# Optimization experiments

Hardware: AMD Instinct MI355X
Metric: run time of the kernel (lower is better)

The kernel has to match this reference:

```python
import jax, jax.numpy as jnp
import numpy as np

B, N, M, K = 128, 20000, 85400, 3  # trajectories, variables, clauses, literals/clause


def setup_inputs() -> dict:
    key = jax.random.key(0)
    k_v, k_idx, k_sign, k_xs = jax.random.split(key, 4)
    v = jax.random.normal(k_v, (B, N), dtype=jnp.float32)
    input_idx = jax.random.randint(k_idx, (B, M, K), 0, N, dtype=jnp.int32)
    # literal signs are exactly +/-1
    input_sign = jnp.where(jax.random.normal(k_sign, (B, M, K)) > 0, 1.0, -1.0).astype(jnp.float32)
    xl = jnp.ones((B, M), dtype=jnp.float32)            # long-term memory (init 1)
    xs = jax.random.uniform(k_xs, (B, M), dtype=jnp.float32)  # short-term memory in [0,1]
    # [alpha, beta, gamma, delta, epsilon, zeta] -- typical MemComputing coefficients
    param = jnp.array([5.0, 20.0, 0.25, 0.05, 0.001, 0.1], dtype=jnp.float32)
    return {"v": v, "xl": xl, "xs": xs, "param": param,
            "input_sign": input_sign, "input_idx": input_idx}


def reference(v, xl, xs, param, input_sign, input_idx):
    """Faithful port of OR.calc_grad. Returns (C, grad_v, dxl, dxs)."""
    b = v.shape[0]
    k = input_idx.shape[-1]
    alpha, beta, gamma, delta, epsilon, zeta = param
    b_idx = jnp.arange(b)[:, None, None]                # (B,1,1)
    inp = v[b_idx, input_idx] * input_sign              # (B,M,K) gather + sign
    v_top, v_top_idx = jax.lax.top_k(inp, 2)            # top-2 literal values per clause
    v_top = (1.0 - v_top) * 0.5                         # transform; v_top[...,0] is smallest -> C
    C = v_top[..., 0]                                   # (B,M) clause 'distance to satisfied'
    hot = jax.nn.one_hot(v_top_idx[..., 0], k, dtype=v.dtype)  # (B,M,K) mask of max literal
    # G: C everywhere, second-best value at the max-literal slot, scaled by xl*xs
    G = jnp.where(hot > 0, v_top[..., 1:2], C[..., None]) * (xl * xs)[..., None]
    # R: C only at the max-literal slot, scaled by (1+zeta*xl)*(1-xs)
    R = hot * C[..., None] * ((1.0 + zeta * xl) * (1.0 - xs))[..., None]
    dv = -(G + R) * input_sign                          # (B,M,K)
    grad_v = jnp.zeros_like(v).at[b_idx, input_idx].add(dv)  # scatter-add over dim 1
    dxl = -alpha * (C - delta)                          # (B,M)
    dxs = -beta * (xs + epsilon) * (C - gamma)          # (B,M)
    return C, grad_v, dxl, dxs
```

## Files before the change

kernel.cpp:

```cpp
#include <hip/hip_runtime.h>


#define NMAX 20000
#define BPB  4

typedef int   int4v   __attribute__((ext_vector_type(4)));
typedef float float4v __attribute__((ext_vector_type(4)));

__device__ __forceinline__ void clause_math(
    float a0, float a1, float a2, float xlv, float xsv, float zeta,
    float& C, float& g0, float& g1, float& g2)
{
    int k0; float m0, m1;
    if (a0 >= a1) {
        if (a0 >= a2) { k0 = 0; m0 = a0; m1 = fmaxf(a1, a2); }
        else          { k0 = 2; m0 = a2; m1 = fmaxf(a0, a1); }
    } else {
        if (a1 >= a2) { k0 = 1; m0 = a1; m1 = fmaxf(a0, a2); }
        else          { k0 = 2; m0 = a2; m1 = fmaxf(a0, a1); }
    }
    C = (1.f - m0) * 0.5f;
    const float T2 = (1.f - m1) * 0.5f;
    const float gl = xlv * xsv;
    const float rC = C * ((1.f + zeta * xlv) * (1.f - xsv));
    g0 = (k0 == 0 ? T2 : C) * gl + (k0 == 0 ? rC : 0.f);
    g1 = (k0 == 1 ? T2 : C) * gl + (k0 == 1 ? rC : 0.f);
    g2 = (k0 == 2 ? T2 : C) * gl + (k0 == 2 ? rC : 0.f);
}

__global__ __launch_bounds__(1024, 8) void or_priv3(
    const float* __restrict__ v,
    const float* __restrict__ xl,
    const float* __restrict__ xs,
    const float* __restrict__ param,
    const float* __restrict__ sign,
    const int*   __restrict__ idx,
    float* __restrict__ outC,
    float* __restrict__ outdxl,
    float* __restrict__ outdxs,
    float* __restrict__ partial,
    int N, int M, int B, int chunk)
{
    __shared__ float sg[NMAX];

    const int id  = blockIdx.x;
    const int cpx = gridDim.x >> 3;
    const int cid = (id & 7) * cpx + (id >> 3);
    const int b   = cid >> 2;
    const int j   = cid & 3;
    const int tid = threadIdx.x;

    {
        float4v* sg4 = (float4v*)sg;
        const float4v z = {0.f, 0.f, 0.f, 0.f};
        const int n4 = N >> 2;
        for (int i = tid; i < n4; i += 1024) sg4[i] = z;
        for (int i = (n4 << 2) + tid; i < N; i += 1024) sg[i] = 0.f;
    }
    __syncthreads();

    const float alpha = param[0], beta = param[1], gamma = param[2];
    const float delta = param[3], eps  = param[4], zeta  = param[5];

    const float* __restrict__ vb = v + (size_t)b * N;

    const int mstart = j * chunk;
    const int mend   = min(M, mstart + chunk);
    const int ngroups = (mend > mstart) ? ((mend - mstart + 3) >> 2) : 0;

    for (int g = tid; g < ngroups; g += 1024) {
        const int m0 = mstart + (g << 2);
        const size_t base = (size_t)b * M + m0;

        if (m0 + 3 < mend) {
            const int4v*   __restrict__ ip = (const int4v*)(idx + base * 3);
            const float4v* __restrict__ sp = (const float4v*)(sign + base * 3);
            const int4v   ia = __builtin_nontemporal_load(ip + 0);
            const int4v   ib = __builtin_nontemporal_load(ip + 1);
            const int4v   ic = __builtin_nontemporal_load(ip + 2);
            const float4v sa = __builtin_nontemporal_load(sp + 0);
            const float4v sb = __builtin_nontemporal_load(sp + 1);
            const float4v sc = __builtin_nontemporal_load(sp + 2);
            const float4v xl4 = __builtin_nontemporal_load((const float4v*)(xl + base));
            const float4v xs4 = __builtin_nontemporal_load((const float4v*)(xs + base));

            const int   ii[12] = {ia.x, ia.y, ia.z, ia.w, ib.x, ib.y, ib.z, ib.w,
                                  ic.x, ic.y, ic.z, ic.w};
            const float ss[12] = {sa.x, sa.y, sa.z, sa.w, sb.x, sb.y, sb.z, sb.w,
                                  sc.x, sc.y, sc.z, sc.w};
            const float xlA[4] = {xl4.x, xl4.y, xl4.z, xl4.w};
            const float xsA[4] = {xs4.x, xs4.y, xs4.z, xs4.w};
            float Cv[4], dxlv[4], dxsv[4];

            #pragma unroll
            for (int c = 0; c < 4; ++c) {
                const int   i0 = ii[3*c], i1 = ii[3*c+1], i2 = ii[3*c+2];
                const float s0 = ss[3*c], s1 = ss[3*c+1], s2 = ss[3*c+2];
                const float a0 = vb[i0] * s0, a1 = vb[i1] * s1, a2 = vb[i2] * s2;
                float C, g0, g1, g2;
                clause_math(a0, a1, a2, xlA[c], xsA[c], zeta, C, g0, g1, g2);
                unsafeAtomicAdd(&sg[i0], -g0 * s0);
                unsafeAtomicAdd(&sg[i1], -g1 * s1);
                unsafeAtomicAdd(&sg[i2], -g2 * s2);
                Cv[c]   = C;
                dxlv[c] = -alpha * (C - delta);
                dxsv[c] = -beta * (xsA[c] + eps) * (C - gamma);
            }
            const float4v cv  = {Cv[0], Cv[1], Cv[2], Cv[3]};
            const float4v lv  = {dxlv[0], dxlv[1], dxlv[2], dxlv[3]};
            const float4v svo = {dxsv[0], dxsv[1], dxsv[2], dxsv[3]};
            __builtin_nontemporal_store(cv,  (float4v*)(outC + base));
            __builtin_nontemporal_store(lv,  (float4v*)(outdxl + base));
            __builtin_nontemporal_store(svo, (float4v*)(outdxs + base));
        } else {
            for (int m = m0; m < mend; ++m) {
                const size_t bm  = (size_t)b * M + m;
                const size_t bm3 = bm * 3;
                const int   i0 = idx[bm3 + 0], i1 = idx[bm3 + 1], i2 = idx[bm3 + 2];
                const float s0 = sign[bm3 + 0], s1 = sign[bm3 + 1], s2 = sign[bm3 + 2];
                const float a0 = vb[i0] * s0, a1 = vb[i1] * s1, a2 = vb[i2] * s2;
                const float xlv = xl[bm], xsv = xs[bm];
                float C, g0, g1, g2;
                clause_math(a0, a1, a2, xlv, xsv, zeta, C, g0, g1, g2);
                unsafeAtomicAdd(&sg[i0], -g0 * s0);
                unsafeAtomicAdd(&sg[i1], -g1 * s1);
                unsafeAtomicAdd(&sg[i2], -g2 * s2);
                outC[bm]   = C;
                outdxl[bm] = -alpha * (C - delta);
                outdxs[bm] = -beta * (xsv + eps) * (C - gamma);
            }
        }
    }
    __syncthreads();

    {
        float* __restrict__ pj = partial + ((size_t)j * B + b) * N;
        const float4v* sg4 = (const float4v*)sg;
        const int n4 = N >> 2;
        for (int i = tid; i < n4; i += 1024)
            __builtin_nontemporal_store(sg4[i], (float4v*)pj + i);
        for (int i = (n4 << 2) + tid; i < N; i += 1024) pj[i] = sg[i];
    }
}

__global__ __launch_bounds__(256) void reduce4(
    const float4v* __restrict__ p, float4v* __restrict__ out, int n4, int stride4)
{
    int i = blockIdx.x * 256 + threadIdx.x;
    const int gs = gridDim.x * 256;
    for (; i < n4; i += gs) {
        const float4v a = p[i];
        const float4v b = p[i + stride4];
        const float4v c = p[i + 2 * stride4];
        const float4v d = p[i + 3 * stride4];
        out[i] = a + b + c + d;
    }
}

__global__ __launch_bounds__(256) void zero_f4(float4v* __restrict__ p, int n4) {
    int i = blockIdx.x * blockDim.x + threadIdx.x;
    int stride = gridDim.x * blockDim.x;
    const float4v z = {0.f, 0.f, 0.f, 0.f};
    for (; i < n4; i += stride) p[i] = z;
}

__global__ __launch_bounds__(256) void or_kernel(
    const float* __restrict__ v, const float* __restrict__ xl,
    const float* __restrict__ xs, const float* __restrict__ param,
    const float* __restrict__ sign, const int* __restrict__ idx,
    float* __restrict__ outC, float* __restrict__ gradv,
    float* __restrict__ outdxl, float* __restrict__ outdxs, int N, int M)
{
    const int m = blockIdx.x * blockDim.x + threadIdx.x;
    const int b = blockIdx.y;
    if (m >= M) return;
    const size_t bm = (size_t)b * M + m;
    const size_t bm3 = bm * 3;
    const int   i0 = idx[bm3 + 0], i1 = idx[bm3 + 1], i2 = idx[bm3 + 2];
    const float s0 = sign[bm3 + 0], s1 = sign[bm3 + 1], s2 = sign[bm3 + 2];
    const float* __restrict__ vb = v + (size_t)b * N;
    const float a0 = vb[i0] * s0, a1 = vb[i1] * s1, a2 = vb[i2] * s2;
    const float xlv = xl[bm], xsv = xs[bm];
    const float alpha = param[0], beta = param[1], gamma = param[2];
    const float delta = param[3], eps  = param[4], zeta  = param[5];

    float C, g0, g1, g2;
    clause_math(a0, a1, a2, xlv, xsv, zeta, C, g0, g1, g2);

    float* __restrict__ gb = gradv + (size_t)b * N;
    atomicAdd(&gb[i0], -g0 * s0);
    atomicAdd(&gb[i1], -g1 * s1);
    atomicAdd(&gb[i2], -g2 * s2);

    outC[bm]   = C;
    outdxl[bm] = -alpha * (C - delta);
    outdxs[bm] = -beta * (xsv + eps) * (C - gamma);
}

extern "C" void kernel_launch(void* const* d_in, const int* in_sizes, int n_in,
                              void* d_out, int out_size, void* d_ws, size_t ws_size,
                              hipStream_t stream) {
    const float* v     = (const float*)d_in[0];
    const float* xl    = (const float*)d_in[1];
    const float* xs    = (const float*)d_in[2];
    const float* param = (const float*)d_in[3];
    const float* sign  = (const float*)d_in[4];
    const int*   idx   = (const int*)d_in[5];

    const int B = 128;
    const int N = in_sizes[0] / B;
    const int M = in_sizes[1] / B;

    float* outC   = (float*)d_out;
    float* gradv  = outC   + (size_t)in_sizes[1];
    float* outdxl = gradv  + (size_t)in_sizes[0];
    float* outdxs = outdxl + (size_t)in_sizes[1];

    const size_t bn = (size_t)B * N;
    const size_t ws_need = (size_t)BPB * bn * sizeof(float);

    if (N <= NMAX && ws_size >= ws_need && (bn % 4) == 0 && (M % 4) == 0) {
        float* partial = (float*)d_ws;
        const int chunk = (((M + BPB - 1) / BPB) + 3) & ~3;
        or_priv3<<<dim3(BPB * B), dim3(1024), 0, stream>>>(
            v, xl, xs, param, sign, idx, outC, outdxl, outdxs,
            (float*)partial, N, M, B, chunk);
        const int n4 = (int)(bn / 4);
        const int rblocks = min(2048, (n4 + 255) / 256);
        reduce4<<<dim3(rblocks), dim3(256), 0, stream>>>(
            (const float4v*)partial, (float4v*)gradv, n4, n4);
    } else {
        const int n4 = (int)(bn / 4);
        zero_f4<<<dim3((n4 + 255) / 256), dim3(256), 0, stream>>>((float4v*)gradv, n4);
        dim3 grid((M + 255) / 256, B);
        or_kernel<<<grid, dim3(256), 0, stream>>>(v, xl, xs, param, sign, idx,
                                                  outC, gradv, outdxl, outdxs, N, M);
    }
}
```

Baseline: 511.2 us.

## Stage v row in LDS, halve clause split per batch, prefetch next clause group

Each block now copies its trajectory's v row into shared memory and gathers from LDS instead of global memory. Clauses per batch are split two ways instead of four, which halves the partial-gradient traffic and the reduction reads. The main loop software-prefetches the next group's idx/sign/xl/xs into registers, and the partial store drops the nontemporal hint. The cost is double the LDS per block (160KB), which likely limits occupancy to one 1024-thread block per CU, and 256 blocks on the device.

```diff
diff --git a/kernel.cpp b/kernel.cpp
--- a/kernel.cpp
+++ b/kernel.cpp
@@ -2,7 +2,7 @@
 
 
 #define NMAX 20000
-#define BPB  4
+#define BPB  2
 
 typedef int   int4v   __attribute__((ext_vector_type(4)));
 typedef float float4v __attribute__((ext_vector_type(4)));
@@ -28,7 +28,7 @@
     g2 = (k0 == 2 ? T2 : C) * gl + (k0 == 2 ? rC : 0.f);
 }
 
-__global__ __launch_bounds__(1024, 8) void or_priv3(
+__global__ __launch_bounds__(1024, 4) void or_priv4(
     const float* __restrict__ v,
     const float* __restrict__ xl,
     const float* __restrict__ xs,
@@ -41,49 +41,77 @@
     float* __restrict__ partial,
     int N, int M, int B, int chunk)
 {
+    __shared__ float sv[NMAX];
     __shared__ float sg[NMAX];
 
     const int id  = blockIdx.x;
     const int cpx = gridDim.x >> 3;
-    const int cid = (id & 7) * cpx + (id >> 3);
-    const int b   = cid >> 2;
-    const int j   = cid & 3;
+    const int cid = ((gridDim.x & 7) == 0) ? ((id & 7) * cpx + (id >> 3)) : id;
+    const int b   = cid >> 1;
+    const int j   = cid & 1;
     const int tid = threadIdx.x;
 
     {
+        const float4v* __restrict__ v4 = (const float4v*)(v + (size_t)b * N);
+        float4v* sv4 = (float4v*)sv;
         float4v* sg4 = (float4v*)sg;
+        const int n4 = N >> 2;
         const float4v z = {0.f, 0.f, 0.f, 0.f};
-        const int n4 = N >> 2;
-        for (int i = tid; i < n4; i += 1024) sg4[i] = z;
-        for (int i = (n4 << 2) + tid; i < N; i += 1024) sg[i] = 0.f;
+        for (int i = tid; i < n4; i += 1024) {
+            sv4[i] = v4[i];
+            sg4[i] = z;
+        }
+        for (int i = (n4 << 2) + tid; i < N; i += 1024) {
+            sv[i] = v[(size_t)b * N + i];
+            sg[i] = 0.f;
+        }
     }
     __syncthreads();
 
     const float alpha = param[0], beta = param[1], gamma = param[2];
     const float delta = param[3], eps  = param[4], zeta  = param[5];
 
-    const float* __restrict__ vb = v + (size_t)b * N;
-
     const int mstart = j * chunk;
     const int mend   = min(M, mstart + chunk);
-    const int ngroups = (mend > mstart) ? ((mend - mstart + 3) >> 2) : 0;
-
-    for (int g = tid; g < ngroups; g += 1024) {
-        const int m0 = mstart + (g << 2);
-        const size_t base = (size_t)b * M + m0;
-
-        if (m0 + 3 < mend) {
+    const int mlen   = mend - mstart;
+
+    if (mlen > 0 && (mlen & 3) == 0) {
+        const int ngroups = mlen >> 2;
+        int g = tid;
+        int4v   ia = {}, ib = {}, ic = {};
+        float4v sa = {}, sb = {}, sc = {}, xl4 = {}, xs4 = {};
+        if (g < ngroups) {
+            const size_t base = (size_t)b * M + mstart + ((size_t)g << 2);
             const int4v*   __restrict__ ip = (const int4v*)(idx + base * 3);
             const float4v* __restrict__ sp = (const float4v*)(sign + base * 3);
-            const int4v   ia = __builtin_nontemporal_load(ip + 0);
-            const int4v   ib = __builtin_nontemporal_load(ip + 1);
-            const int4v   ic = __builtin_nontemporal_load(ip + 2);
-            const float4v sa = __builtin_nontemporal_load(sp + 0);
-            const float4v sb = __builtin_nontemporal_load(sp + 1);
-            const float4v sc = __builtin_nontemporal_load(sp + 2);
-            const float4v xl4 = __builtin_nontemporal_load((const float4v*)(xl + base));
-            const float4v xs4 = __builtin_nontemporal_load((const float4v*)(xs + base));
-
+            ia = __builtin_nontemporal_load(ip + 0);
+            ib = __builtin_nontemporal_load(ip + 1);
+            ic = __builtin_nontemporal_load(ip + 2);
+            sa = __builtin_nontemporal_load(sp + 0);
+            sb = __builtin_nontemporal_load(sp + 1);
+            sc = __builtin_nontemporal_load(sp + 2);
+            xl4 = __builtin_nontemporal_load((const float4v*)(xl + base));
+            xs4 = __builtin_nontemporal_load((const float4v*)(xs + base));
+        }
+        for (; g < ngroups; g += 1024) {
+            const int gn = g + 1024;
+            int4v   ia2 = {}, ib2 = {}, ic2 = {};
+            float4v sa2 = {}, sb2 = {}, sc2 = {}, xl42 = {}, xs42 = {};
+            if (gn < ngroups) {
+                const size_t basen = (size_t)b * M + mstart + ((size_t)gn << 2);
+                const int4v*   __restrict__ ipn = (const int4v*)(idx + basen * 3);
+                const float4v* __restrict__ spn = (const float4v*)(sign + basen * 3);
+                ia2 = __builtin_nontemporal_load(ipn + 0);
+                ib2 = __builtin_nontemporal_load(ipn + 1);
+                ic2 = __builtin_nontemporal_load(ipn + 2);
+                sa2 = __builtin_nontemporal_load(spn + 0);
+                sb2 = __builtin_nontemporal_load(spn + 1);
+                sc2 = __builtin_nontemporal_load(spn + 2);
+                xl42 = __builtin_nontemporal_load((const float4v*)(xl + basen));
+                xs42 = __builtin_nontemporal_load((const float4v*)(xs + basen));
+            }
+
+            const size_t base = (size_t)b * M + mstart + ((size_t)g << 2);
             const int   ii[12] = {ia.x, ia.y, ia.z, ia.w, ib.x, ib.y, ib.z, ib.w,
                                   ic.x, ic.y, ic.z, ic.w};
             const float ss[12] = {sa.x, sa.y, sa.z, sa.w, sb.x, sb.y, sb.z, sb.w,
@@ -96,7 +124,7 @@
             for (int c = 0; c < 4; ++c) {
                 const int   i0 = ii[3*c], i1 = ii[3*c+1], i2 = ii[3*c+2];
                 const float s0 = ss[3*c], s1 = ss[3*c+1], s2 = ss[3*c+2];
-                const float a0 = vb[i0] * s0, a1 = vb[i1] * s1, a2 = vb[i2] * s2;
+                const float a0 = sv[i0] * s0, a1 = sv[i1] * s1, a2 = sv[i2] * s2;
                 float C, g0, g1, g2;
                 clause_math(a0, a1, a2, xlA[c], xsA[c], zeta, C, g0, g1, g2);
                 unsafeAtomicAdd(&sg[i0], -g0 * s0);
@@ -112,23 +140,27 @@
             __builtin_nontemporal_store(cv,  (float4v*)(outC + base));
             __builtin_nontemporal_store(lv,  (float4v*)(outdxl + base));
             __builtin_nontemporal_store(svo, (float4v*)(outdxs + base));
-        } else {
-            for (int m = m0; m < mend; ++m) {
-                const size_t bm  = (size_t)b * M + m;
-                const size_t bm3 = bm * 3;
-                const int   i0 = idx[bm3 + 0], i1 = idx[bm3 + 1], i2 = idx[bm3 + 2];
-                const float s0 = sign[bm3 + 0], s1 = sign[bm3 + 1], s2 = sign[bm3 + 2];
-                const float a0 = vb[i0] * s0, a1 = vb[i1] * s1, a2 = vb[i2] * s2;
-                const float xlv = xl[bm], xsv = xs[bm];
-                float C, g0, g1, g2;
-                clause_math(a0, a1, a2, xlv, xsv, zeta, C, g0, g1, g2);
-                unsafeAtomicAdd(&sg[i0], -g0 * s0);
-                unsafeAtomicAdd(&sg[i1], -g1 * s1);
-                unsafeAtomicAdd(&sg[i2], -g2 * s2);
-                outC[bm]   = C;
-                outdxl[bm] = -alpha * (C - delta);
-                outdxs[bm] = -beta * (xsv + eps) * (C - gamma);
-            }
+
+            ia = ia2; ib = ib2; ic = ic2;
+            sa = sa2; sb = sb2; sc = sc2;
+            xl4 = xl42; xs4 = xs42;
+        }
+    } else {
+        for (int m = mstart + tid; m < mend; m += 1024) {
+            const size_t bm  = (size_t)b * M + m;
+            const size_t bm3 = bm * 3;
+            const int   i0 = idx[bm3 + 0], i1 = idx[bm3 + 1], i2 = idx[bm3 + 2];
+            const float s0 = sign[bm3 + 0], s1 = sign[bm3 + 1], s2 = sign[bm3 + 2];
+            const float a0 = sv[i0] * s0, a1 = sv[i1] * s1, a2 = sv[i2] * s2;
+            const float xlv = xl[bm], xsv = xs[bm];
+            float C, g0, g1, g2;
+            clause_math(a0, a1, a2, xlv, xsv, zeta, C, g0, g1, g2);
+            unsafeAtomicAdd(&sg[i0], -g0 * s0);
+            unsafeAtomicAdd(&sg[i1], -g1 * s1);
+            unsafeAtomicAdd(&sg[i2], -g2 * s2);
+            outC[bm]   = C;
+            outdxl[bm] = -alpha * (C - delta);
+            outdxs[bm] = -beta * (xsv + eps) * (C - gamma);
         }
     }
     __syncthreads();
@@ -138,12 +170,12 @@
         const float4v* sg4 = (const float4v*)sg;
         const int n4 = N >> 2;
         for (int i = tid; i < n4; i += 1024)
-            __builtin_nontemporal_store(sg4[i], (float4v*)pj + i);
+            ((float4v*)pj)[i] = sg4[i];
         for (int i = (n4 << 2) + tid; i < N; i += 1024) pj[i] = sg[i];
     }
 }
 
-__global__ __launch_bounds__(256) void reduce4(
+__global__ __launch_bounds__(256) void reduce2(
     const float4v* __restrict__ p, float4v* __restrict__ out, int n4, int stride4)
 {
     int i = blockIdx.x * 256 + threadIdx.x;
@@ -151,9 +183,7 @@
     for (; i < n4; i += gs) {
         const float4v a = p[i];
         const float4v b = p[i + stride4];
-        const float4v c = p[i + 2 * stride4];
-        const float4v d = p[i + 3 * stride4];
-        out[i] = a + b + c + d;
+        out[i] = a + b;
     }
 }
 
@@ -222,12 +252,12 @@
     if (N <= NMAX && ws_size >= ws_need && (bn % 4) == 0 && (M % 4) == 0) {
         float* partial = (float*)d_ws;
         const int chunk = (((M + BPB - 1) / BPB) + 3) & ~3;
-        or_priv3<<<dim3(BPB * B), dim3(1024), 0, stream>>>(
+        or_priv4<<<dim3(BPB * B), dim3(1024), 0, stream>>>(
             v, xl, xs, param, sign, idx, outC, outdxl, outdxs,
             (float*)partial, N, M, B, chunk);
         const int n4 = (int)(bn / 4);
         const int rblocks = min(2048, (n4 + 255) / 256);
-        reduce4<<<dim3(rblocks), dim3(256), 0, stream>>>(
+        reduce2<<<dim3(rblocks), dim3(256), 0, stream>>>(
             (const float4v*)partial, (float4v*)gradv, n4, n4);
     } else {
         const int n4 = (int)(bn / 4);
```

After: 461.7 us. 9.7% less time.
